# Kernel tuning notes

Measured on AMD Instinct MI355X. Metric: run time of the kernel, lower is better.

## Reference

```python
import jax, jax.numpy as jnp
import numpy as np

S = 3        # message passing steps
L = 128      # latent size
N = 10000    # nodes
E = 160000   # edges
DN, DE, DG = 64, 16, 8
OUT = 8
EPS = 1e-5


def _ln(x, scale, offset):
    m = jnp.mean(x, axis=-1, keepdims=True)
    v = jnp.var(x, axis=-1, keepdims=True)
    return (x - m) * jax.lax.rsqrt(v + EPS) * scale + offset


def _mlp(x, W0, b0, W1, b1):
    h = jax.nn.relu(x @ W0 + b0)
    return jax.nn.relu(h @ W1 + b1)


def setup_inputs() -> dict:
    key = jax.random.key(0)
    ks = iter(jax.random.split(key, 64))

    def w(shape, fan_in):
        return jax.random.normal(next(ks), shape, jnp.float32) / np.sqrt(fan_in).astype(np.float32)

    inp = {
        "nodes": jax.random.normal(next(ks), (N, DN), jnp.float32),
        "edges": jax.random.normal(next(ks), (E, DE), jnp.float32),
        "globals_": jax.random.normal(next(ks), (1, DG), jnp.float32),
        "senders": jax.random.randint(next(ks), (E,), 0, N),
        "receivers": jax.random.randint(next(ks), (E,), 0, N),
        # embedder
        "emb_node_W": w((DN, L), DN), "emb_node_b": jnp.zeros((L,), jnp.float32),
        "emb_edge_W": w((DE, L), DE), "emb_edge_b": jnp.zeros((L,), jnp.float32),
        "emb_glob_W": w((DG, L), DG), "emb_glob_b": jnp.zeros((L,), jnp.float32),
        # per-step MLPs (2 layers each)
        "edge_W0": w((S, 4 * L, L), 4 * L), "edge_b0": jnp.zeros((S, L), jnp.float32),
        "edge_W1": w((S, L, L), L),         "edge_b1": jnp.zeros((S, L), jnp.float32),
        "node_W0": w((S, 4 * L, L), 4 * L), "node_b0": jnp.zeros((S, L), jnp.float32),
        "node_W1": w((S, L, L), L),         "node_b1": jnp.zeros((S, L), jnp.float32),
        "glob_W0": w((S, 3 * L, L), 3 * L), "glob_b0": jnp.zeros((S, L), jnp.float32),
        "glob_W1": w((S, L, L), L),         "glob_b1": jnp.zeros((S, L), jnp.float32),
        # per-step layernorm (0: nodes, 1: edges, 2: globals)
        "ln_scale": jnp.ones((S, 3, L), jnp.float32),
        "ln_offset": jnp.zeros((S, 3, L), jnp.float32),
        # decoder (globals only)
        "dec_W": w((L, OUT), L), "dec_b": jnp.zeros((OUT,), jnp.float32),
    }
    return inp


def reference(nodes, edges, globals_, senders, receivers,
              emb_node_W, emb_node_b, emb_edge_W, emb_edge_b, emb_glob_W, emb_glob_b,
              edge_W0, edge_b0, edge_W1, edge_b1,
              node_W0, node_b0, node_W1, node_b1,
              glob_W0, glob_b0, glob_W1, glob_b1,
              ln_scale, ln_offset, dec_W, dec_b):
    # embed to latent
    n = nodes @ emb_node_W + emb_node_b      # [N, L]
    e = edges @ emb_edge_W + emb_edge_b      # [E, L]
    g = globals_ @ emb_glob_W + emb_glob_b   # [1, L]

    for s in range(S):
        # edge update: concat(edges, nodes[senders], nodes[receivers], globals)
        g_e = jnp.broadcast_to(g, (e.shape[0], L))
        e_in = jnp.concatenate([e, n[senders], n[receivers], g_e], axis=-1)  # [E, 4L]
        e_new = _mlp(e_in, edge_W0[s], edge_b0[s], edge_W1[s], edge_b1[s])
        # node update: concat(nodes, segsum(e,senders), segsum(e,receivers), globals)
        sent_agg = jax.ops.segment_sum(e_new, senders, num_segments=N)
        recv_agg = jax.ops.segment_sum(e_new, receivers, num_segments=N)
        g_n = jnp.broadcast_to(g, (N, L))
        n_in = jnp.concatenate([n, sent_agg, recv_agg, g_n], axis=-1)  # [N, 4L]
        n_new = _mlp(n_in, node_W0[s], node_b0[s], node_W1[s], node_b1[s])
        # global update: concat(node_agg, edge_agg, globals) (single graph)
        node_agg = jnp.sum(n_new, axis=0, keepdims=True)
        edge_agg = jnp.sum(e_new, axis=0, keepdims=True)
        g_in = jnp.concatenate([node_agg, edge_agg, g], axis=-1)  # [1, 3L]
        g_new = _mlp(g_in, glob_W0[s], glob_b0[s], glob_W1[s], glob_b1[s])
        # residual + layernorm
        n = _ln(n_new + n, ln_scale[s, 0], ln_offset[s, 0])
        e = _ln(e_new + e, ln_scale[s, 1], ln_offset[s, 1])
        g = _ln(g_new + g, ln_scale[s, 2], ln_offset[s, 2])

    # decoder maps globals only
    return g @ dec_W + dec_b  # [1, OUT]
```

## Files before the change

### kernel.cpp

```cpp
#include <hip/hip_runtime.h>
#include <hip/hip_bf16.h>

typedef __bf16 bf16;
typedef __bf16 bf16x8 __attribute__((ext_vector_type(8)));
typedef __bf16 bf16x4 __attribute__((ext_vector_type(4)));
typedef float  f32x4  __attribute__((ext_vector_type(4)));

#define NL 128
#define NN 10000
#define NE 160000
#define LN_EPS 1e-5f

__device__ __forceinline__ f32x4 f4zero() {
    f32x4 v; v[0] = 0.f; v[1] = 0.f; v[2] = 0.f; v[3] = 0.f; return v;
}

__device__ __forceinline__ int swz_off(int row, int b) {
    return row * 256 + (b ^ ((row & 7) << 4));
}

__device__ __forceinline__ bf16x8 frag_ld(const bf16* base, int row, int kbyte) {
    return *reinterpret_cast<const bf16x8*>(
        reinterpret_cast<const char*>(base) + swz_off(row, kbyte));
}

template <int NT>
__device__ __forceinline__ void stage_img(const bf16* __restrict__ img, bf16* dst, int tid) {
    #pragma unroll
    for (int i = 0; i < 2048 / NT; ++i) {
        int byte = (i * NT + tid) * 16;
        *reinterpret_cast<bf16x8*>(reinterpret_cast<char*>(dst) + byte) =
            *reinterpret_cast<const bf16x8*>(reinterpret_cast<const char*>(img) + byte);
    }
}

template <int NT>
__device__ __forceinline__ void stage_img_ld(const bf16* __restrict__ img, bf16x8* r, int tid) {
    #pragma unroll
    for (int i = 0; i < 2048 / NT; ++i)
        r[i] = *reinterpret_cast<const bf16x8*>(reinterpret_cast<const char*>(img) +
                                                (i * NT + tid) * 16);
}
template <int NT>
__device__ __forceinline__ void stage_img_st(bf16* dst, const bf16x8* r, int tid) {
    #pragma unroll
    for (int i = 0; i < 2048 / NT; ++i)
        *reinterpret_cast<bf16x8*>(reinterpret_cast<char*>(dst) + (i * NT + tid) * 16) = r[i];
}

__device__ __forceinline__ void stage_rows16(const float* __restrict__ src0, bf16* sX,
                                             int wrow0, int lane) {
    int c8 = (lane & 15) * 8;
    #pragma unroll
    for (int i = 0; i < 4; ++i) {
        int sub = i * 4 + (lane >> 4);
        const float* src = src0 + (size_t)sub * 128 + c8;
        f32x4 a = *reinterpret_cast<const f32x4*>(src);
        f32x4 b = *reinterpret_cast<const f32x4*>(src + 4);
        bf16x8 v;
        v[0] = (bf16)a[0]; v[1] = (bf16)a[1]; v[2] = (bf16)a[2]; v[3] = (bf16)a[3];
        v[4] = (bf16)b[0]; v[5] = (bf16)b[1]; v[6] = (bf16)b[2]; v[7] = (bf16)b[3];
        *reinterpret_cast<bf16x8*>(reinterpret_cast<char*>(sX) + swz_off(wrow0 + sub, c8 * 2)) = v;
    }
}

__device__ __forceinline__ void mfma_16x128(const bf16* sA, const bf16* sB, int arow, int kq,
                                            f32x4 acc[8]) {
    #pragma unroll
    for (int kk = 0; kk < 4; ++kk) {
        bf16x8 af = frag_ld(sA, arow, kk * 64 + kq);
        #pragma unroll
        for (int t = 0; t < 8; ++t) {
            bf16x8 bfr = frag_ld(sB, t * 16 + (arow & 15), kk * 64 + kq);
            acc[t] = __builtin_amdgcn_mfma_f32_16x16x32_bf16(af, bfr, acc[t], 0, 0, 0);
        }
    }
}

__device__ __forceinline__ void acc_to_lds_bf16(bf16* sX, const f32x4 acc[8], int w, int lane) {
    int c0 = lane & 15;
    #pragma unroll
    for (int r = 0; r < 4; ++r) {
        int rl = w * 16 + (lane >> 4) * 4 + r;
        #pragma unroll
        for (int t = 0; t < 8; ++t) {
            int col = t * 16 + c0;
            *reinterpret_cast<bf16*>(reinterpret_cast<char*>(sX) + swz_off(rl, col * 2)) =
                (bf16)acc[t][r];
        }
    }
}

__device__ __forceinline__ void lds_rows_to_global_bf16(const bf16* sX, bf16* __restrict__ dst0,
                                                        int w, int lane) {
    int c8 = (lane & 15) * 8;
    #pragma unroll
    for (int i = 0; i < 4; ++i) {
        int sub = i * 4 + (lane >> 4);
        bf16x8 v = *reinterpret_cast<const bf16x8*>(
            reinterpret_cast<const char*>(sX) + swz_off(w * 16 + sub, c8 * 2));
        *reinterpret_cast<bf16x8*>(dst0 + (size_t)sub * 128 + c8) = v;
    }
}

__global__ void k_prep(const float* __restrict__ eW0, const float* __restrict__ eW1,
                       const float* __restrict__ nW0, const float* __restrict__ nW1,
                       bf16* __restrict__ imgs, const float* __restrict__ globals_,
                       const float* __restrict__ embW, const float* __restrict__ embB,
                       float* __restrict__ g, const float* __restrict__ eb0,
                       const float* __restrict__ nb0, float* __restrict__ gve,
                       float* __restrict__ gvn, int* __restrict__ deg,
                       float* __restrict__ eagg, float* __restrict__ nagg,
                       int* __restrict__ done) {
    const int b = blockIdx.x;
    const int tid = threadIdx.x;
    if (b < 24) {
        const int s = b >> 3, kind = b & 7;
        const float* src;
        if (kind < 3)       src = eW0 + (size_t)s * 512 * 128 + (size_t)kind * 128 * 128;
        else if (kind == 3) src = eW1 + (size_t)s * 128 * 128;
        else if (kind < 7)  src = nW0 + (size_t)s * 512 * 128 + (size_t)(kind - 4) * 128 * 128;
        else                src = nW1 + (size_t)s * 128 * 128;
        bf16* img = imgs + (size_t)b * 16384;
        for (int i = 0; i < 16; ++i) {
            int q = tid + i * 256;
            int col = q & 127;
            int k0 = (q >> 7) << 2;
            bf16x4 v;
            v[0] = (bf16)src[(k0 + 0) * 128 + col];
            v[1] = (bf16)src[(k0 + 1) * 128 + col];
            v[2] = (bf16)src[(k0 + 2) * 128 + col];
            v[3] = (bf16)src[(k0 + 3) * 128 + col];
            *reinterpret_cast<bf16x4*>(reinterpret_cast<char*>(img) + swz_off(col, k0 * 2)) = v;
        }
    } else if (b == 24) {
        __shared__ float sG[128];
        if (tid < 3) done[tid] = 0;
        if (tid < 128) {
            float a = embB[tid];
            #pragma unroll
            for (int k = 0; k < 8; ++k) a += globals_[k] * embW[k * 128 + tid];
            g[tid] = a;
            sG[tid] = a;
        }
        __syncthreads();
        if (tid < 128) {
            const float* eW0g = eW0 + 384 * 128;
            const float* nW0g = nW0 + 384 * 128;
            float ae = eb0[tid], an = nb0[tid];
            for (int k = 0; k < 128; ++k) {
                float gv = sG[k];
                ae += gv * eW0g[k * 128 + tid];
                an += gv * nW0g[k * 128 + tid];
            }
            gve[tid] = ae;
            gvn[tid] = an;
        }
    } else {
        for (int i = tid; i < 2 * NN; i += 256) deg[i] = 0;
        for (int i = tid; i < 8 * 128; i += 256) eagg[i] = 0.f;
        for (int i = tid; i < 4 * 128; i += 256) nagg[i] = 0.f;
    }
}


__global__ void k_hist(const int* __restrict__ senders, const int* __restrict__ receivers,
                       int* __restrict__ deg_s, int* __restrict__ deg_r) {
    int i = blockIdx.x * 256 + threadIdx.x;
    if (i < NE) {
        atomicAdd(&deg_s[senders[i]], 1);
        atomicAdd(&deg_r[receivers[i]], 1);
    }
}

__device__ void scan_arr(const int* __restrict__ deg, int* __restrict__ rs, int* __restrict__ cur,
                         int* sW, int* sRun) {
    const int tid = threadIdx.x, lane = tid & 63, wid = tid >> 6;
    if (tid == 0) *sRun = 0;
    __syncthreads();
    for (int base = 0; base < NN; base += 1024) {
        int i = base + tid;
        int orig = (i < NN) ? deg[i] : 0;
        int v = orig;
        #pragma unroll
        for (int off = 1; off < 64; off <<= 1) {
            int u = __shfl_up(v, off, 64);
            if (lane >= off) v += u;
        }
        if (lane == 63) sW[wid] = v;
        __syncthreads();
        if (wid == 0 && lane < 16) {
            int u = sW[lane];
            #pragma unroll
            for (int off = 1; off < 16; off <<= 1) {
                int t = __shfl_up(u, off, 16);
                if (lane >= off) u += t;
            }
            sW[lane] = u;
        }
        __syncthreads();
        int waveoff = (wid == 0) ? 0 : sW[wid - 1];
        int incl = v + waveoff + *sRun;
        if (i < NN) {
            rs[i + 1] = incl;
            cur[i] = incl - orig;
        }
        __syncthreads();
        if (tid == 1023) *sRun = incl;
        __syncthreads();
    }
    if (tid == 0) rs[0] = 0;
}

__global__ void k_scan(const int* __restrict__ deg_s, int* __restrict__ rs_s,
                       int* __restrict__ cur_s, const int* __restrict__ deg_r,
                       int* __restrict__ rs_r, int* __restrict__ cur_r) {
    __shared__ int sW[16];
    __shared__ int sRun;
    scan_arr(deg_s, rs_s, cur_s, sW, &sRun);
    __syncthreads();
    scan_arr(deg_r, rs_r, cur_r, sW, &sRun);
}

__global__ void k_scatter_s(const int* __restrict__ senders, const int* __restrict__ receivers,
                            int* __restrict__ cur_s, int* __restrict__ perm,
                            int* __restrict__ snd_s, int* __restrict__ rcv_s) {
    int i = blockIdx.x * 256 + threadIdx.x;
    if (i < NE) {
        int s = senders[i];
        int p = atomicAdd(&cur_s[s], 1);
        perm[p] = i;
        snd_s[p] = s;
        rcv_s[p] = receivers[i];
    }
}

__global__ void k_scatter_r(const int* __restrict__ rcv_s, int* __restrict__ cur_r,
                            int* __restrict__ csr_r) {
    int j = blockIdx.x * 256 + threadIdx.x;
    if (j < NE) {
        int r = rcv_s[j];
        int p = atomicAdd(&cur_r[r], 1);
        csr_r[p] = j;
    }
}


__global__ __launch_bounds__(256, 2) void k_embed_nodes(
    const float* __restrict__ nodes, const float* __restrict__ W, const float* __restrict__ b,
    float* __restrict__ n_out, const bf16* __restrict__ imgPs, const bf16* __restrict__ imgPr,
    bf16* __restrict__ nsW, bf16* __restrict__ nrW) {
    __shared__ __align__(16) char smem[81920];
    float* sWemb = (float*)smem;
    float* sB = (float*)(smem + 32768);
    bf16* sWa = (bf16*)smem;
    bf16* sWb = (bf16*)(smem + 32768);
    bf16* sX = (bf16*)(smem + 65536);
    const int tid = threadIdx.x;
    const int lane = tid & 63;
    const int w = tid >> 6;
    const int rowbase = blockIdx.x * 64;
    const bool wvalid = (rowbase + w * 16) < NN;

    for (int i = tid; i < 64 * 128; i += 256) sWemb[i] = W[i];
    if (tid < 128) sB[tid] = b[tid];
    __syncthreads();

    const int rg = tid >> 4;
    const int c8 = (tid & 15) * 8;
    #pragma unroll
    for (int p = 0; p < 4; ++p) {
        int row = rowbase + p * 16 + rg;
        if (row < NN) {
            const f32x4* x4 = reinterpret_cast<const f32x4*>(nodes + (size_t)row * 64);
            float o[8];
            #pragma unroll
            for (int j = 0; j < 8; ++j) o[j] = sB[c8 + j];
            #pragma unroll
            for (int k4 = 0; k4 < 16; ++k4) {
                f32x4 xv = x4[k4];
                #pragma unroll
                for (int kk = 0; kk < 4; ++kk) {
                    float x = xv[kk];
                    const float* wrow = sWemb + (k4 * 4 + kk) * 128 + c8;
                    f32x4 wA = *reinterpret_cast<const f32x4*>(wrow);
                    f32x4 wB = *reinterpret_cast<const f32x4*>(wrow + 4);
                    o[0] += x * wA[0]; o[1] += x * wA[1]; o[2] += x * wA[2]; o[3] += x * wA[3];
                    o[4] += x * wB[0]; o[5] += x * wB[1]; o[6] += x * wB[2]; o[7] += x * wB[3];
                }
            }
            f32x4 oA, oB;
            bf16x8 v;
            #pragma unroll
            for (int j = 0; j < 8; ++j) {
                if (j < 4) oA[j] = o[j]; else oB[j - 4] = o[j];
                v[j] = (bf16)o[j];
            }
            float* orow = n_out + (size_t)row * 128 + c8;
            *reinterpret_cast<f32x4*>(orow) = oA;
            *reinterpret_cast<f32x4*>(orow + 4) = oB;
            *reinterpret_cast<bf16x8*>(reinterpret_cast<char*>(sX) +
                                       swz_off(p * 16 + rg, c8 * 2)) = v;
        }
    }
    __syncthreads();
    stage_img<256>(imgPs, sWa, tid);
    stage_img<256>(imgPr, sWb, tid);
    __syncthreads();
    if (!wvalid) return;

    const int arow = w * 16 + (lane & 15);
    const int kq = (lane >> 4) * 16;
    f32x4 acc[8], acc2[8];
    #pragma unroll
    for (int t = 0; t < 8; ++t) { acc[t] = f4zero(); acc2[t] = f4zero(); }
    mfma_16x128(sX, sWa, arow, kq, acc);
    mfma_16x128(sX, sWb, arow, kq, acc2);

    acc_to_lds_bf16(sX, acc, w, lane);
    lds_rows_to_global_bf16(sX, nsW + (size_t)(rowbase + w * 16) * 128, w, lane);
    acc_to_lds_bf16(sX, acc2, w, lane);
    lds_rows_to_global_bf16(sX, nrW + (size_t)(rowbase + w * 16) * 128, w, lane);
}

__global__ __launch_bounds__(256) void k_embed_edges(const float* __restrict__ edges,
                                                     const int* __restrict__ perm,
                                                     const float* __restrict__ W,
                                                     const float* __restrict__ b,
                                                     bf16* __restrict__ e_out) {
    __shared__ float sW[16 * 128];
    __shared__ float sB[128];
    const int tid = threadIdx.x;
    for (int i = tid; i < 16 * 128; i += 256) sW[i] = W[i];
    if (tid < 128) sB[tid] = b[tid];
    __syncthreads();
    const int rg = tid >> 4;
    const int c8 = (tid & 15) * 8;
    const int rowbase = blockIdx.x * 128;
    #pragma unroll 2
    for (int p = 0; p < 8; ++p) {
        int row = rowbase + p * 16 + rg;
        int src = perm[row];
        const f32x4* x4 = reinterpret_cast<const f32x4*>(edges + (size_t)src * 16);
        f32x4 xr[4] = {x4[0], x4[1], x4[2], x4[3]};
        float o[8];
        #pragma unroll
        for (int j = 0; j < 8; ++j) o[j] = sB[c8 + j];
        #pragma unroll
        for (int q = 0; q < 4; ++q) {
            #pragma unroll
            for (int kk = 0; kk < 4; ++kk) {
                float x = xr[q][kk];
                const float* wrow = sW + (q * 4 + kk) * 128 + c8;
                f32x4 wA = *reinterpret_cast<const f32x4*>(wrow);
                f32x4 wB = *reinterpret_cast<const f32x4*>(wrow + 4);
                o[0] += x * wA[0]; o[1] += x * wA[1]; o[2] += x * wA[2]; o[3] += x * wA[3];
                o[4] += x * wB[0]; o[5] += x * wB[1]; o[6] += x * wB[2]; o[7] += x * wB[3];
            }
        }
        bf16x8 v;
        #pragma unroll
        for (int j = 0; j < 8; ++j) v[j] = (bf16)o[j];
        *reinterpret_cast<bf16x8*>(e_out + (size_t)row * 128 + c8) = v;
    }
}


__global__ __launch_bounds__(512, 2) void k_edge(
    bf16* e_rw, bf16* __restrict__ e_new_out, const bf16* __restrict__ nsW,
    const bf16* __restrict__ nrW, float* __restrict__ edge_agg,
    const int* __restrict__ snd_s, const int* __restrict__ rcv_s,
    const bf16* __restrict__ imgW0, const bf16* __restrict__ imgW1,
    const float* __restrict__ gvec, const float* __restrict__ b1,
    const float* __restrict__ lnS, const float* __restrict__ lnO) {
    __shared__ __align__(16) char smem[65536];
    bf16* sW = (bf16*)smem;
    bf16* sX = (bf16*)(smem + 32768);
    float* sEagg = (float*)smem;

    const int tid = threadIdx.x;
    const int lane = tid & 63;
    const int w = tid >> 6;
    const int rowbase = blockIdx.x * 128;
    const int arow = w * 16 + (lane & 15);
    const int kq = (lane >> 4) * 16;
    const int c0 = lane & 15;
    const int qrt = lane >> 4;
    const int c8 = c0 * 8;

    stage_img<512>(imgW0, sW, tid);

    int snd_i[4], rcv_i[4];
    bf16x8 eold8[4];
    #pragma unroll
    for (int i = 0; i < 4; ++i) {
        int gr = rowbase + w * 16 + i * 4 + qrt;
        snd_i[i] = snd_s[gr];
        rcv_i[i] = rcv_s[gr];
        eold8[i] = *reinterpret_cast<const bf16x8*>(e_rw + (size_t)gr * 128 + c8);
    }

    f32x4 gvA = *reinterpret_cast<const f32x4*>(gvec + c8);
    f32x4 gvB = *reinterpret_cast<const f32x4*>(gvec + c8 + 4);
    f32x4 lsA = *reinterpret_cast<const f32x4*>(lnS + c8);
    f32x4 lsB = *reinterpret_cast<const f32x4*>(lnS + c8 + 4);
    f32x4 loA = *reinterpret_cast<const f32x4*>(lnO + c8);
    f32x4 loB = *reinterpret_cast<const f32x4*>(lnO + c8 + 4);
    float bb[8];
    #pragma unroll
    for (int t = 0; t < 8; ++t) bb[t] = b1[t * 16 + c0];

    bf16x8 ns8[4], nr8[4];
    #pragma unroll
    for (int i = 0; i < 4; ++i) {
        ns8[i] = *reinterpret_cast<const bf16x8*>(nsW + (size_t)snd_i[i] * 128 + c8);
        nr8[i] = *reinterpret_cast<const bf16x8*>(nrW + (size_t)rcv_i[i] * 128 + c8);
    }

    #pragma unroll
    for (int i = 0; i < 4; ++i)
        *reinterpret_cast<bf16x8*>(reinterpret_cast<char*>(sX) +
                                   swz_off(w * 16 + i * 4 + qrt, c8 * 2)) = eold8[i];

    __syncthreads();

    f32x4 acc[8];
    #pragma unroll
    for (int t = 0; t < 8; ++t) acc[t] = f4zero();
    __builtin_amdgcn_s_setprio(1);
    mfma_16x128(sX, sW, arow, kq, acc);
    __builtin_amdgcn_s_setprio(0);

    __syncthreads();

    bf16x8 w1r[4];
    stage_img_ld<512>(imgW1, w1r, tid);

    #pragma unroll
    for (int r = 0; r < 4; ++r) {
        int rl = w * 16 + (lane >> 4) * 4 + r;
        #pragma unroll
        for (int t = 0; t < 8; ++t)
            *reinterpret_cast<bf16*>(reinterpret_cast<char*>(sX) +
                                     swz_off(rl, (t * 16 + c0) * 2)) = (bf16)acc[t][r];
    }
    #pragma unroll
    for (int i = 0; i < 4; ++i) {
        int rl = w * 16 + i * 4 + qrt;
        bf16x8 a8 = *reinterpret_cast<const bf16x8*>(
            reinterpret_cast<const char*>(sX) + swz_off(rl, c8 * 2));
        bf16x8 h8;
        #pragma unroll
        for (int j = 0; j < 8; ++j) {
            float gvj = (j < 4) ? gvA[j] : gvB[j - 4];
            float v = (float)a8[j] + (float)ns8[i][j] + (float)nr8[i][j] + gvj;
            h8[j] = (bf16)fmaxf(v, 0.f);
        }
        *reinterpret_cast<bf16x8*>(reinterpret_cast<char*>(sX) + swz_off(rl, c8 * 2)) = h8;
    }

    stage_img_st<512>(sW, w1r, tid);
    __syncthreads();

    f32x4 acc2[8];
    #pragma unroll
    for (int t = 0; t < 8; ++t) acc2[t] = f4zero();
    __builtin_amdgcn_s_setprio(1);
    mfma_16x128(sX, sW, arow, kq, acc2);
    __builtin_amdgcn_s_setprio(0);

    #pragma unroll
    for (int r = 0; r < 4; ++r) {
        int rl = w * 16 + (lane >> 4) * 4 + r;
        #pragma unroll
        for (int t = 0; t < 8; ++t)
            *reinterpret_cast<bf16*>(reinterpret_cast<char*>(sX) +
                                     swz_off(rl, (t * 16 + c0) * 2)) =
                (bf16)fmaxf(acc2[t][r] + bb[t], 0.f);
    }

    float cs[8];
    #pragma unroll
    for (int j = 0; j < 8; ++j) cs[j] = 0.f;
    bf16* enew0 = e_new_out + (size_t)rowbase * 128;
    bf16* e0 = e_rw + (size_t)rowbase * 128;
    #pragma unroll
    for (int i = 0; i < 4; ++i) {
        int sub = w * 16 + i * 4 + qrt;
        bf16x8 en8 = *reinterpret_cast<const bf16x8*>(
            reinterpret_cast<const char*>(sX) + swz_off(sub, c8 * 2));
        *reinterpret_cast<bf16x8*>(enew0 + (size_t)sub * 128 + c8) = en8;
        float rv[8], s1 = 0.f, s2 = 0.f;
        #pragma unroll
        for (int j = 0; j < 8; ++j) {
            float en = (float)en8[j];
            cs[j] += en;
            float v = en + (float)eold8[i][j];
            rv[j] = v;
            s1 += v;
            s2 += v * v;
        }
        #pragma unroll
        for (int off = 1; off < 16; off <<= 1) {
            s1 += __shfl_xor(s1, off, 16);
            s2 += __shfl_xor(s2, off, 16);
        }
        float mean = s1 * (1.f / 128.f);
        float rstd = rsqrtf(s2 * (1.f / 128.f) - mean * mean + LN_EPS);
        bf16x8 o8;
        #pragma unroll
        for (int j = 0; j < 8; ++j) {
            float ls = (j < 4) ? lsA[j] : lsB[j - 4];
            float lo = (j < 4) ? loA[j] : loB[j - 4];
            o8[j] = (bf16)((rv[j] - mean) * rstd * ls + lo);
        }
        *reinterpret_cast<bf16x8*>(e0 + (size_t)sub * 128 + c8) = o8;
    }

    #pragma unroll
    for (int j = 0; j < 8; ++j) {
        cs[j] += __shfl_xor(cs[j], 16, 64);
        cs[j] += __shfl_xor(cs[j], 32, 64);
    }
    __syncthreads();
    if (qrt == 0) {
        float* dst = sEagg + w * 128 + c8;
        #pragma unroll
        for (int j = 0; j < 8; ++j) dst[j] = cs[j];
    }
    __syncthreads();
    if (tid < 128) {
        float v = 0.f;
        #pragma unroll
        for (int ww = 0; ww < 8; ++ww) v += sEagg[ww * 128 + tid];
        atomicAdd(&edge_agg[(blockIdx.x & 7) * 128 + tid], v);
    }
}

__global__ __launch_bounds__(256) void k_agg(const bf16* __restrict__ e_new,
                                             const int* __restrict__ rs_s,
                                             const int* __restrict__ rs_r,
                                             const int* __restrict__ csr_r,
                                             bf16* __restrict__ sent, bf16* __restrict__ recv) {
    const int lane = threadIdx.x & 63;
    const int w = threadIdx.x >> 6;
    const int node = blockIdx.x * 4 + w;
    if (node >= NN) return;
    const int qrt = lane >> 4;
    const int c8 = (lane & 15) * 8;
    float a[8];
    #pragma unroll
    for (int j = 0; j < 8; ++j) a[j] = 0.f;
    const int b0 = rs_s[node], b1 = rs_s[node + 1];
    for (int jj = b0 + qrt; jj < b1; jj += 4) {
        bf16x8 v = *reinterpret_cast<const bf16x8*>(e_new + (size_t)jj * 128 + c8);
        #pragma unroll
        for (int j = 0; j < 8; ++j) a[j] += (float)v[j];
    }
    #pragma unroll
    for (int j = 0; j < 8; ++j) {
        a[j] += __shfl_xor(a[j], 16, 64);
        a[j] += __shfl_xor(a[j], 32, 64);
    }
    if (qrt == 0) {
        bf16x8 o;
        #pragma unroll
        for (int j = 0; j < 8; ++j) o[j] = (bf16)a[j];
        *reinterpret_cast<bf16x8*>(sent + (size_t)node * 128 + c8) = o;
    }
    #pragma unroll
    for (int j = 0; j < 8; ++j) a[j] = 0.f;
    const int c1 = rs_r[node], c2 = rs_r[node + 1];
    for (int pp = c1 + qrt; pp < c2; pp += 4) {
        int jj = csr_r[pp];
        bf16x8 v = *reinterpret_cast<const bf16x8*>(e_new + (size_t)jj * 128 + c8);
        #pragma unroll
        for (int j = 0; j < 8; ++j) a[j] += (float)v[j];
    }
    #pragma unroll
    for (int j = 0; j < 8; ++j) {
        a[j] += __shfl_xor(a[j], 16, 64);
        a[j] += __shfl_xor(a[j], 32, 64);
    }
    if (qrt == 0) {
        bf16x8 o;
        #pragma unroll
        for (int j = 0; j < 8; ++j) o[j] = (bf16)a[j];
        *reinterpret_cast<bf16x8*>(recv + (size_t)node * 128 + c8) = o;
    }
}

__global__ __launch_bounds__(256, 2) void k_node(
    float* n_rw, const bf16* __restrict__ sent, const bf16* __restrict__ recv,
    float* __restrict__ node_agg , const bf16* __restrict__ imgW0,
    const bf16* __restrict__ imgW1, const float* __restrict__ gvec,
    const float* __restrict__ b1, const float* __restrict__ lnS,
    const float* __restrict__ lnO, const bf16* __restrict__ imgPs,
    const bf16* __restrict__ imgPr, bf16* __restrict__ nsW, bf16* __restrict__ nrW,
    int do_proj,
    int* __restrict__ done_ctr, float* __restrict__ edge_agg , float* __restrict__ g,
    const float* __restrict__ gW0, const float* __restrict__ gb0,
    const float* __restrict__ gW1, const float* __restrict__ gb1,
    const float* __restrict__ glnS, const float* __restrict__ glnO,
    const float* __restrict__ eW0g, const float* __restrict__ eb0n,
    const float* __restrict__ nW0g, const float* __restrict__ nb0n,
    float* __restrict__ gve, float* __restrict__ gvn, const float* __restrict__ decW,
    const float* __restrict__ decb, float* __restrict__ out, int do_next, int do_dec) {
    __shared__ __align__(16) char smem[81920];
    __shared__ int sLast;
    bf16* sA = (bf16*)smem;
    bf16* sB = (bf16*)(smem + 32768);
    bf16* sX = (bf16*)(smem + 65536);
    float* sNagg = (float*)smem;

    const int tid = threadIdx.x;
    const int lane = tid & 63;
    const int w = tid >> 6;
    const int rowbase = blockIdx.x * 64;
    const bool wvalid = (rowbase + w * 16) < NN;
    const int arow = w * 16 + (lane & 15);
    const int kq = (lane >> 4) * 16;
    const int c0 = lane & 15;
    const int qrt = lane >> 4;
    const int c8 = c0 * 8;

    stage_img<256>(imgW0, sA, tid);
    stage_img<256>(imgW0 + 16384, sB, tid);
    bf16x8 sent8[4], recv8[4];
    if (wvalid) {
        stage_rows16(n_rw + (size_t)(rowbase + w * 16) * 128, sX, w * 16, lane);
        #pragma unroll
        for (int i = 0; i < 4; ++i) {
            int gr = rowbase + w * 16 + i * 4 + qrt;
            sent8[i] = *reinterpret_cast<const bf16x8*>(sent + (size_t)gr * 128 + c8);
            recv8[i] = *reinterpret_cast<const bf16x8*>(recv + (size_t)gr * 128 + c8);
        }
    }
    __syncthreads();

    float gvf[8], bbf[8];
    #pragma unroll
    for (int t = 0; t < 8; ++t) {
        gvf[t] = gvec[t * 16 + c0];
        bbf[t] = b1[t * 16 + c0];
    }
    f32x4 lsA4 = *reinterpret_cast<const f32x4*>(lnS + c8);
    f32x4 lsB4 = *reinterpret_cast<const f32x4*>(lnS + c8 + 4);
    f32x4 loA4 = *reinterpret_cast<const f32x4*>(lnO + c8);
    f32x4 loB4 = *reinterpret_cast<const f32x4*>(lnO + c8 + 4);

    f32x4 acc[8];
    #pragma unroll
    for (int t = 0; t < 8; ++t) acc[t] = f4zero();
    float cs[8];
    #pragma unroll
    for (int j = 0; j < 8; ++j) cs[j] = 0.f;

    if (wvalid) mfma_16x128(sX, sA, arow, kq, acc);
    __syncthreads();

    stage_img<256>(imgW0 + 32768, sA, tid);
    if (wvalid) {
        #pragma unroll
        for (int i = 0; i < 4; ++i)
            *reinterpret_cast<bf16x8*>(reinterpret_cast<char*>(sX) +
                                       swz_off(w * 16 + i * 4 + qrt, c8 * 2)) = sent8[i];
        mfma_16x128(sX, sB, arow, kq, acc);
    }
    __syncthreads();

    stage_img<256>(imgW1, sB, tid);
    if (wvalid) {
        #pragma unroll
        for (int i = 0; i < 4; ++i)
            *reinterpret_cast<bf16x8*>(reinterpret_cast<char*>(sX) +
                                       swz_off(w * 16 + i * 4 + qrt, c8 * 2)) = recv8[i];
        mfma_16x128(sX, sA, arow, kq, acc);

        #pragma unroll
        for (int r = 0; r < 4; ++r) {
            int rl = w * 16 + (lane >> 4) * 4 + r;
            #pragma unroll
            for (int t = 0; t < 8; ++t)
                *reinterpret_cast<bf16*>(reinterpret_cast<char*>(sX) +
                                         swz_off(rl, (t * 16 + c0) * 2)) =
                    (bf16)fmaxf(acc[t][r] + gvf[t], 0.f);
        }
    }
    __syncthreads();

    if (wvalid) {
        #pragma unroll
        for (int t = 0; t < 8; ++t) acc[t] = f4zero();
        mfma_16x128(sX, sB, arow, kq, acc);
        #pragma unroll
        for (int r = 0; r < 4; ++r) {
            int rl = w * 16 + (lane >> 4) * 4 + r;
            #pragma unroll
            for (int t = 0; t < 8; ++t)
                *reinterpret_cast<bf16*>(reinterpret_cast<char*>(sX) +
                                         swz_off(rl, (t * 16 + c0) * 2)) =
                    (bf16)fmaxf(acc[t][r] + bbf[t], 0.f);
        }

        const float* nbase = n_rw + (size_t)(rowbase + w * 16) * 128;
        #pragma unroll
        for (int i = 0; i < 4; ++i) {
            int sub = i * 4 + qrt;
            bf16x8 en8 = *reinterpret_cast<const bf16x8*>(
                reinterpret_cast<const char*>(sX) + swz_off(w * 16 + sub, c8 * 2));
            f32x4 noA = *reinterpret_cast<const f32x4*>(nbase + (size_t)sub * 128 + c8);
            f32x4 noB = *reinterpret_cast<const f32x4*>(nbase + (size_t)sub * 128 + c8 + 4);
            float rv[8], s1 = 0.f, s2 = 0.f;
            #pragma unroll
            for (int j = 0; j < 8; ++j) {
                float en = (float)en8[j];
                cs[j] += en;
                float v = en + ((j < 4) ? noA[j] : noB[j - 4]);
                rv[j] = v;
                s1 += v;
                s2 += v * v;
            }
            #pragma unroll
            for (int off = 1; off < 16; off <<= 1) {
                s1 += __shfl_xor(s1, off, 16);
                s2 += __shfl_xor(s2, off, 16);
            }
            float mean = s1 * (1.f / 128.f);
            float rstd = rsqrtf(s2 * (1.f / 128.f) - mean * mean + LN_EPS);
            f32x4 oA, oB;
            bf16x8 l8;
            #pragma unroll
            for (int j = 0; j < 8; ++j) {
                float ls = (j < 4) ? lsA4[j] : lsB4[j - 4];
                float lo = (j < 4) ? loA4[j] : loB4[j - 4];
                float o = (rv[j] - mean) * rstd * ls + lo;
                if (j < 4) oA[j] = o; else oB[j - 4] = o;
                l8[j] = (bf16)o;
            }
            float* orow = n_rw + (size_t)(rowbase + w * 16 + sub) * 128 + c8;
            *reinterpret_cast<f32x4*>(orow) = oA;
            *reinterpret_cast<f32x4*>(orow + 4) = oB;
            *reinterpret_cast<bf16x8*>(reinterpret_cast<char*>(sX) +
                                       swz_off(w * 16 + sub, c8 * 2)) = l8;
        }
    }

    if (do_proj) {
        __syncthreads();
        stage_img<256>(imgPs, sA, tid);
        stage_img<256>(imgPr, sB, tid);
        __syncthreads();
        if (wvalid) {
            f32x4 pa[8], pb[8];
            #pragma unroll
            for (int t = 0; t < 8; ++t) { pa[t] = f4zero(); pb[t] = f4zero(); }
            mfma_16x128(sX, sA, arow, kq, pa);
            mfma_16x128(sX, sB, arow, kq, pb);
            acc_to_lds_bf16(sX, pa, w, lane);
            lds_rows_to_global_bf16(sX, nsW + (size_t)(rowbase + w * 16) * 128, w, lane);
            acc_to_lds_bf16(sX, pb, w, lane);
            lds_rows_to_global_bf16(sX, nrW + (size_t)(rowbase + w * 16) * 128, w, lane);
        }
    }

    #pragma unroll
    for (int j = 0; j < 8; ++j) {
        cs[j] += __shfl_xor(cs[j], 16, 64);
        cs[j] += __shfl_xor(cs[j], 32, 64);
    }
    __syncthreads();
    if (qrt == 0) {
        float* dst = sNagg + w * 128 + c8;
        #pragma unroll
        for (int j = 0; j < 8; ++j) dst[j] = wvalid ? cs[j] : 0.f;
    }
    __syncthreads();
    if (tid < 128) {
        float v = sNagg[tid] + sNagg[128 + tid] + sNagg[256 + tid] + sNagg[384 + tid];
        atomicAdd(&node_agg[(blockIdx.x & 3) * 128 + tid], v);
    }

    __syncthreads();
    if (tid == 0) {
        __threadfence();
        int old = atomicAdd(done_ctr, 1);
        sLast = (old == (int)gridDim.x - 1);
    }
    __syncthreads();
    if (!sLast) return;

    float* sIn = (float*)smem;
    float* sP0 = sIn + 384;
    float* sP1 = sP0 + 128;
    float* sH = sP1 + 128;
    float* sG = sH + 128;
    float* sMR = sG + 128;
    const int j = tid & 127;
    const int part = tid >> 7;

    if (tid < 128) {
        float v = 0.f;
        #pragma unroll
        for (int c = 0; c < 4; ++c) v += atomicAdd(&node_agg[c * 128 + tid], 0.f);
        #pragma unroll
        for (int c = 0; c < 4; ++c) atomicExch(&node_agg[c * 128 + tid], 0.f);
        sIn[tid] = v;
        sIn[256 + tid] = g[tid];
    } else {
        float v = 0.f;
        #pragma unroll
        for (int c = 0; c < 8; ++c) v += edge_agg[c * 128 + j];
        #pragma unroll
        for (int c = 0; c < 8; ++c) edge_agg[c * 128 + j] = 0.f;
        sIn[128 + j] = v;
    }
    __syncthreads();
    {
        float p = 0.f;
        for (int k = 0; k < 192; ++k) {
            int kk = part * 192 + k;
            p += sIn[kk] * gW0[(size_t)kk * 128 + j];
        }
        (part ? sP1 : sP0)[j] = p;
    }
    __syncthreads();
    if (tid < 128) sH[tid] = fmaxf(gb0[tid] + sP0[tid] + sP1[tid], 0.f);
    __syncthreads();
    {
        float p = 0.f;
        for (int k = 0; k < 64; ++k) {
            int kk = part * 64 + k;
            p += sH[kk] * gW1[(size_t)kk * 128 + j];
        }
        (part ? sP1 : sP0)[j] = p;
    }
    __syncthreads();
    float res = 0.f;
    if (tid < 128) {
        res = fmaxf(gb1[tid] + sP0[tid] + sP1[tid], 0.f) + sIn[256 + tid];
        sP0[tid] = res;
        sP1[tid] = res * res;
    }
    __syncthreads();
    if (tid < 64) {
        float a = sP0[tid] + sP0[tid + 64];
        float q = sP1[tid] + sP1[tid + 64];
        #pragma unroll
        for (int off = 1; off < 64; off <<= 1) {
            a += __shfl_xor(a, off, 64);
            q += __shfl_xor(q, off, 64);
        }
        if (tid == 0) {
            float m = a * (1.f / 128.f);
            float v = q * (1.f / 128.f) - m * m;
            sMR[0] = m;
            sMR[1] = rsqrtf(v + LN_EPS);
        }
    }
    __syncthreads();
    if (tid < 128) {
        float go = (res - sMR[0]) * sMR[1] * glnS[tid] + glnO[tid];
        g[tid] = go;
        sG[tid] = go;
    }
    __syncthreads();
    if (do_next) {
        float pe = 0.f, pn = 0.f;
        for (int k = 0; k < 64; ++k) {
            int kk = part * 64 + k;
            float gv = sG[kk];
            pe += gv * eW0g[(size_t)kk * 128 + j];
            pn += gv * nW0g[(size_t)kk * 128 + j];
        }
        (part ? sP1 : sP0)[j] = pe;
        sIn[part * 128 + j] = pn;
        __syncthreads();
        if (tid < 128) {
            gve[tid] = eb0n[tid] + sP0[tid] + sP1[tid];
            gvn[tid] = nb0n[tid] + sIn[tid] + sIn[128 + tid];
        }
    }
    if (do_dec && tid < 8) {
        float a = decb[tid];
        for (int k = 0; k < 128; ++k) a += sG[k] * decW[k * 8 + tid];
        out[tid] = a;
    }
}

extern "C" void kernel_launch(void* const* d_in, const int* in_sizes, int n_in, void* d_out,
                              int out_size, void* d_ws, size_t ws_size, hipStream_t stream) {
    (void)in_sizes; (void)n_in; (void)out_size; (void)ws_size;
    const float* nodes = (const float*)d_in[0];
    const float* edges = (const float*)d_in[1];
    const float* globals_ = (const float*)d_in[2];
    const int* senders = (const int*)d_in[3];
    const int* receivers = (const int*)d_in[4];
    const float* emb_node_W = (const float*)d_in[5];
    const float* emb_node_b = (const float*)d_in[6];
    const float* emb_edge_W = (const float*)d_in[7];
    const float* emb_edge_b = (const float*)d_in[8];
    const float* emb_glob_W = (const float*)d_in[9];
    const float* emb_glob_b = (const float*)d_in[10];
    const float* edge_W0 = (const float*)d_in[11];
    const float* edge_b0 = (const float*)d_in[12];
    const float* edge_W1 = (const float*)d_in[13];
    const float* edge_b1 = (const float*)d_in[14];
    const float* node_W0 = (const float*)d_in[15];
    const float* node_b0 = (const float*)d_in[16];
    const float* node_W1 = (const float*)d_in[17];
    const float* node_b1 = (const float*)d_in[18];
    const float* glob_W0 = (const float*)d_in[19];
    const float* glob_b0 = (const float*)d_in[20];
    const float* glob_W1 = (const float*)d_in[21];
    const float* glob_b1 = (const float*)d_in[22];
    const float* ln_scale = (const float*)d_in[23];
    const float* ln_offset = (const float*)d_in[24];
    const float* dec_W = (const float*)d_in[25];
    const float* dec_b = (const float*)d_in[26];

    char* ws = (char*)d_ws;
    size_t off = 0;
    auto alloc = [&](size_t bytes) -> char* {
        char* p = ws + off;
        off += (bytes + 255) & ~(size_t)255;
        return p;
    };
    bf16* e = (bf16*)alloc((size_t)NE * NL * 2);
    bf16* e_new = (bf16*)alloc((size_t)NE * NL * 2);
    float* n = (float*)alloc((size_t)NN * NL * 4);
    bf16* nsW = (bf16*)alloc((size_t)NN * NL * 2);
    bf16* nrW = (bf16*)alloc((size_t)NN * NL * 2);
    bf16* sent = (bf16*)alloc((size_t)NN * NL * 2);
    bf16* recv = (bf16*)alloc((size_t)NN * NL * 2);
    bf16* imgs = (bf16*)alloc((size_t)24 * 16384 * 2);
    float* eagg = (float*)alloc(8 * 128 * 4);
    float* nagg = (float*)alloc(4 * 128 * 4);
    float* g = (float*)alloc(128 * 4);
    float* gve = (float*)alloc(128 * 4);
    float* gvn = (float*)alloc(128 * 4);
    int* done = (int*)alloc(16 * 4);
    int* deg = (int*)alloc((size_t)2 * NN * 4);
    int* deg_s = deg;
    int* deg_r = deg + NN;
    int* rs_s = (int*)alloc((size_t)(NN + 1) * 4);
    int* rs_r = (int*)alloc((size_t)(NN + 1) * 4);
    int* cur_s = (int*)alloc((size_t)NN * 4);
    int* cur_r = (int*)alloc((size_t)NN * 4);
    int* perm = (int*)alloc((size_t)NE * 4);
    int* snd_s = (int*)alloc((size_t)NE * 4);
    int* rcv_s = (int*)alloc((size_t)NE * 4);
    int* csr_r = (int*)alloc((size_t)NE * 4);

    const int NB_N = (NN + 63) / 64;
    const int NB_E = NE / 128;
    const int NB_EMB = NE / 128;
    const int NB_SC = (NE + 255) / 256;
    const int NB_AGG = NN / 4;

    auto img = [&](int s, int kind) -> const bf16* {
        return imgs + ((size_t)s * 8 + kind) * 16384;
    };

    k_prep<<<26, 256, 0, stream>>>(edge_W0, edge_W1, node_W0, node_W1, imgs, globals_,
                                   emb_glob_W, emb_glob_b, g, edge_b0, node_b0, gve, gvn,
                                   deg, eagg, nagg, done);

    k_hist<<<NB_SC, 256, 0, stream>>>(senders, receivers, deg_s, deg_r);
    k_scan<<<1, 1024, 0, stream>>>(deg_s, rs_s, cur_s, deg_r, rs_r, cur_r);
    k_scatter_s<<<NB_SC, 256, 0, stream>>>(senders, receivers, cur_s, perm, snd_s, rcv_s);
    k_scatter_r<<<NB_SC, 256, 0, stream>>>(rcv_s, cur_r, csr_r);

    k_embed_nodes<<<NB_N, 256, 0, stream>>>(nodes, emb_node_W, emb_node_b, n, img(0, 1),
                                            img(0, 2), nsW, nrW);
    k_embed_edges<<<NB_EMB, 256, 0, stream>>>(edges, perm, emb_edge_W, emb_edge_b, e);

    for (int s = 0; s < 3; ++s) {
        const int last = (s == 2);
        k_edge<<<NB_E, 512, 0, stream>>>(e, e_new, nsW, nrW, eagg, snd_s, rcv_s, img(s, 0),
                                         img(s, 3), gve, edge_b1 + s * 128,
                                         ln_scale + (s * 3 + 1) * 128,
                                         ln_offset + (s * 3 + 1) * 128);
        k_agg<<<NB_AGG, 256, 0, stream>>>(e_new, rs_s, rs_r, csr_r, sent, recv);
        const float* eW0g = last ? edge_W0 : edge_W0 + (size_t)(s + 1) * 512 * 128 + 384 * 128;
        const float* eb0n = last ? edge_b0 : edge_b0 + (s + 1) * 128;
        const float* nW0g = last ? node_W0 : node_W0 + (size_t)(s + 1) * 512 * 128 + 384 * 128;
        const float* nb0n = last ? node_b0 : node_b0 + (s + 1) * 128;
        k_node<<<NB_N, 256, 0, stream>>>(
            n, sent, recv, nagg, img(s, 4), img(s, 7), gvn, node_b1 + s * 128,
            ln_scale + (s * 3 + 0) * 128, ln_offset + (s * 3 + 0) * 128,
            img(last ? 0 : s + 1, 1), img(last ? 0 : s + 1, 2), nsW, nrW, !last,
            done + s, eagg, g, glob_W0 + (size_t)s * 384 * 128, glob_b0 + s * 128,
            glob_W1 + (size_t)s * 128 * 128, glob_b1 + s * 128, ln_scale + (s * 3 + 2) * 128,
            ln_offset + (s * 3 + 2) * 128, eW0g, eb0n, nW0g, nb0n, gve, gvn, dec_W, dec_b,
            (float*)d_out, !last, last);
    }
}
```

Before: 400.4 us.

## Read edge MLP weights as MFMA fragments from global instead of staging in LDS

Adds a prep step that stores the edge MLP weights pre-arranged in MFMA B-fragment order, so each lane reads its fragment straight from global memory (through L2 and cache) rather than staging a 32KB weight tile in LDS. The edge kernel shrinks to 256 threads handling 64 rows per block, with far less LDS and fewer block-wide barriers, which should allow more resident blocks and better latency hiding. The cost is that every wave now fetches the full weight matrices from global or cache, so performance depends on cache hit rates.

```diff
diff --git a/kernel.cpp b/kernel.cpp
--- a/kernel.cpp
+++ b/kernel.cpp
@@ -32,20 +32,6 @@
         *reinterpret_cast<bf16x8*>(reinterpret_cast<char*>(dst) + byte) =
             *reinterpret_cast<const bf16x8*>(reinterpret_cast<const char*>(img) + byte);
     }
-}
-
-template <int NT>
-__device__ __forceinline__ void stage_img_ld(const bf16* __restrict__ img, bf16x8* r, int tid) {
-    #pragma unroll
-    for (int i = 0; i < 2048 / NT; ++i)
-        r[i] = *reinterpret_cast<const bf16x8*>(reinterpret_cast<const char*>(img) +
-                                                (i * NT + tid) * 16);
-}
-template <int NT>
-__device__ __forceinline__ void stage_img_st(bf16* dst, const bf16x8* r, int tid) {
-    #pragma unroll
-    for (int i = 0; i < 2048 / NT; ++i)
-        *reinterpret_cast<bf16x8*>(reinterpret_cast<char*>(dst) + (i * NT + tid) * 16) = r[i];
 }
 
 __device__ __forceinline__ void stage_rows16(const float* __restrict__ src0, bf16* sX,
@@ -77,6 +63,20 @@
     }
 }
 
+__device__ __forceinline__ void mfma_16x128g(const bf16* sA, const bf16* __restrict__ imgB,
+                                             int arow, int kq, int lane, f32x4 acc[8]) {
+    #pragma unroll
+    for (int kk = 0; kk < 4; ++kk) {
+        bf16x8 af = frag_ld(sA, arow, kk * 64 + kq);
+        #pragma unroll
+        for (int t = 0; t < 8; ++t) {
+            bf16x8 bfr = *reinterpret_cast<const bf16x8*>(
+                imgB + (size_t)(((kk * 8 + t) * 64 + lane)) * 8);
+            acc[t] = __builtin_amdgcn_mfma_f32_16x16x32_bf16(af, bfr, acc[t], 0, 0, 0);
+        }
+    }
+}
+
 __device__ __forceinline__ void acc_to_lds_bf16(bf16* sX, const f32x4 acc[8], int w, int lane) {
     int c0 = lane & 15;
     #pragma unroll
@@ -105,7 +105,8 @@
 
 __global__ void k_prep(const float* __restrict__ eW0, const float* __restrict__ eW1,
                        const float* __restrict__ nW0, const float* __restrict__ nW1,
-                       bf16* __restrict__ imgs, const float* __restrict__ globals_,
+                       bf16* __restrict__ imgs, bf16* __restrict__ fimgs,
+                       const float* __restrict__ globals_,
                        const float* __restrict__ embW, const float* __restrict__ embB,
                        float* __restrict__ g, const float* __restrict__ eb0,
                        const float* __restrict__ nb0, float* __restrict__ gve,
@@ -133,7 +134,25 @@
             v[3] = (bf16)src[(k0 + 3) * 128 + col];
             *reinterpret_cast<bf16x4*>(reinterpret_cast<char*>(img) + swz_off(col, k0 * 2)) = v;
         }
-    } else if (b == 24) {
+    } else if (b < 30) {
+        const int f = b - 24, s = f >> 1, which = f & 1;
+        const float* src = which ? (eW1 + (size_t)s * 128 * 128)
+                                 : (eW0 + (size_t)s * 512 * 128);
+        bf16* img = fimgs + (size_t)f * 16384;
+        #pragma unroll
+        for (int i = 0; i < 8; ++i) {
+            int q = tid + i * 256;
+            int l = q & 63;
+            int ft = q >> 6;
+            int kk = ft >> 3, t = ft & 7;
+            int col = t * 16 + (l & 15);
+            int k0 = kk * 32 + (l >> 4) * 8;
+            bf16x8 v;
+            #pragma unroll
+            for (int j = 0; j < 8; ++j) v[j] = (bf16)src[(size_t)(k0 + j) * 128 + col];
+            *reinterpret_cast<bf16x8*>(img + (size_t)q * 8) = v;
+        }
+    } else if (b == 30) {
         __shared__ float sG[128];
         if (tid < 3) done[tid] = 0;
         if (tid < 128) {
@@ -366,30 +385,27 @@
 }
 
 
-__global__ __launch_bounds__(512, 2) void k_edge(
+__global__ __launch_bounds__(256) void k_edge(
     bf16* e_rw, bf16* __restrict__ e_new_out, const bf16* __restrict__ nsW,
     const bf16* __restrict__ nrW, float* __restrict__ edge_agg,
     const int* __restrict__ snd_s, const int* __restrict__ rcv_s,
-    const bf16* __restrict__ imgW0, const bf16* __restrict__ imgW1,
+    const bf16* __restrict__ fimgW0, const bf16* __restrict__ fimgW1,
     const float* __restrict__ gvec, const float* __restrict__ b1,
     const float* __restrict__ lnS, const float* __restrict__ lnO) {
-    __shared__ __align__(16) char smem[65536];
-    bf16* sW = (bf16*)smem;
-    bf16* sX = (bf16*)(smem + 32768);
-    float* sEagg = (float*)smem;
+    __shared__ __align__(16) char smem[18432];
+    bf16* sX = (bf16*)smem;
+    float* sEagg = (float*)(smem + 16384);
 
     const int tid = threadIdx.x;
     const int lane = tid & 63;
     const int w = tid >> 6;
-    const int rowbase = blockIdx.x * 128;
+    const int rowbase = blockIdx.x * 64;
     const int arow = w * 16 + (lane & 15);
     const int kq = (lane >> 4) * 16;
     const int c0 = lane & 15;
     const int qrt = lane >> 4;
     const int c8 = c0 * 8;
 
-    stage_img<512>(imgW0, sW, tid);
-
     int snd_i[4], rcv_i[4];
     bf16x8 eold8[4];
     #pragma unroll
@@ -399,46 +415,30 @@
         rcv_i[i] = rcv_s[gr];
         eold8[i] = *reinterpret_cast<const bf16x8*>(e_rw + (size_t)gr * 128 + c8);
     }
-
-    f32x4 gvA = *reinterpret_cast<const f32x4*>(gvec + c8);
-    f32x4 gvB = *reinterpret_cast<const f32x4*>(gvec + c8 + 4);
-    f32x4 lsA = *reinterpret_cast<const f32x4*>(lnS + c8);
-    f32x4 lsB = *reinterpret_cast<const f32x4*>(lnS + c8 + 4);
-    f32x4 loA = *reinterpret_cast<const f32x4*>(lnO + c8);
-    f32x4 loB = *reinterpret_cast<const f32x4*>(lnO + c8 + 4);
-    float bb[8];
-    #pragma unroll
-    for (int t = 0; t < 8; ++t) bb[t] = b1[t * 16 + c0];
-
     bf16x8 ns8[4], nr8[4];
     #pragma unroll
     for (int i = 0; i < 4; ++i) {
         ns8[i] = *reinterpret_cast<const bf16x8*>(nsW + (size_t)snd_i[i] * 128 + c8);
         nr8[i] = *reinterpret_cast<const bf16x8*>(nrW + (size_t)rcv_i[i] * 128 + c8);
     }
+    f32x4 gvA = *reinterpret_cast<const f32x4*>(gvec + c8);
+    f32x4 gvB = *reinterpret_cast<const f32x4*>(gvec + c8 + 4);
 
     #pragma unroll
     for (int i = 0; i < 4; ++i)
         *reinterpret_cast<bf16x8*>(reinterpret_cast<char*>(sX) +
                                    swz_off(w * 16 + i * 4 + qrt, c8 * 2)) = eold8[i];
 
-    __syncthreads();
-
     f32x4 acc[8];
     #pragma unroll
     for (int t = 0; t < 8; ++t) acc[t] = f4zero();
     __builtin_amdgcn_s_setprio(1);
-    mfma_16x128(sX, sW, arow, kq, acc);
+    mfma_16x128g(sX, fimgW0, arow, kq, lane, acc);
     __builtin_amdgcn_s_setprio(0);
 
-    __syncthreads();
-
-    bf16x8 w1r[4];
-    stage_img_ld<512>(imgW1, w1r, tid);
-
     #pragma unroll
     for (int r = 0; r < 4; ++r) {
-        int rl = w * 16 + (lane >> 4) * 4 + r;
+        int rl = w * 16 + qrt * 4 + r;
         #pragma unroll
         for (int t = 0; t < 8; ++t)
             *reinterpret_cast<bf16*>(reinterpret_cast<char*>(sX) +
@@ -459,19 +459,24 @@
         *reinterpret_cast<bf16x8*>(reinterpret_cast<char*>(sX) + swz_off(rl, c8 * 2)) = h8;
     }
 
-    stage_img_st<512>(sW, w1r, tid);
-    __syncthreads();
-
     f32x4 acc2[8];
     #pragma unroll
     for (int t = 0; t < 8; ++t) acc2[t] = f4zero();
     __builtin_amdgcn_s_setprio(1);
-    mfma_16x128(sX, sW, arow, kq, acc2);
+    mfma_16x128g(sX, fimgW1, arow, kq, lane, acc2);
     __builtin_amdgcn_s_setprio(0);
 
+    float bb[8];
+    #pragma unroll
+    for (int t = 0; t < 8; ++t) bb[t] = b1[t * 16 + c0];
+    f32x4 lsA = *reinterpret_cast<const f32x4*>(lnS + c8);
+    f32x4 lsB = *reinterpret_cast<const f32x4*>(lnS + c8 + 4);
+    f32x4 loA = *reinterpret_cast<const f32x4*>(lnO + c8);
+    f32x4 loB = *reinterpret_cast<const f32x4*>(lnO + c8 + 4);
+
     #pragma unroll
     for (int r = 0; r < 4; ++r) {
-        int rl = w * 16 + (lane >> 4) * 4 + r;
+        int rl = w * 16 + qrt * 4 + r;
         #pragma unroll
         for (int t = 0; t < 8; ++t)
             *reinterpret_cast<bf16*>(reinterpret_cast<char*>(sX) +
@@ -530,9 +535,7 @@
     }
     __syncthreads();
     if (tid < 128) {
-        float v = 0.f;
-        #pragma unroll
-        for (int ww = 0; ww < 8; ++ww) v += sEagg[ww * 128 + tid];
+        float v = sEagg[tid] + sEagg[128 + tid] + sEagg[256 + tid] + sEagg[384 + tid];
         atomicAdd(&edge_agg[(blockIdx.x & 7) * 128 + tid], v);
     }
 }
@@ -934,6 +937,7 @@
     bf16* sent = (bf16*)alloc((size_t)NN * NL * 2);
     bf16* recv = (bf16*)alloc((size_t)NN * NL * 2);
     bf16* imgs = (bf16*)alloc((size_t)24 * 16384 * 2);
+    bf16* fimgs = (bf16*)alloc((size_t)6 * 16384 * 2);
     float* eagg = (float*)alloc(8 * 128 * 4);
     float* nagg = (float*)alloc(4 * 128 * 4);
     float* g = (float*)alloc(128 * 4);
@@ -953,7 +957,7 @@
     int* csr_r = (int*)alloc((size_t)NE * 4);
 
     const int NB_N = (NN + 63) / 64;
-    const int NB_E = NE / 128;
+    const int NB_E = NE / 64;
     const int NB_EMB = NE / 128;
     const int NB_SC = (NE + 255) / 256;
     const int NB_AGG = NN / 4;
@@ -961,8 +965,11 @@
     auto img = [&](int s, int kind) -> const bf16* {
         return imgs + ((size_t)s * 8 + kind) * 16384;
     };
-
-    k_prep<<<26, 256, 0, stream>>>(edge_W0, edge_W1, node_W0, node_W1, imgs, globals_,
+    auto fimg = [&](int s, int which) -> const bf16* {
+        return fimgs + ((size_t)s * 2 + which) * 16384;
+    };
+
+    k_prep<<<32, 256, 0, stream>>>(edge_W0, edge_W1, node_W0, node_W1, imgs, fimgs, globals_,
                                    emb_glob_W, emb_glob_b, g, edge_b0, node_b0, gve, gvn,
                                    deg, eagg, nagg, done);
 
@@ -977,8 +984,8 @@
 
     for (int s = 0; s < 3; ++s) {
         const int last = (s == 2);
-        k_edge<<<NB_E, 512, 0, stream>>>(e, e_new, nsW, nrW, eagg, snd_s, rcv_s, img(s, 0),
-                                         img(s, 3), gve, edge_b1 + s * 128,
+        k_edge<<<NB_E, 256, 0, stream>>>(e, e_new, nsW, nrW, eagg, snd_s, rcv_s, fimg(s, 0),
+                                         fimg(s, 1), gve, edge_b1 + s * 128,
                                          ln_scale + (s * 3 + 1) * 128,
                                          ln_offset + (s * 3 + 1) * 128);
         k_agg<<<NB_AGG, 256, 0, stream>>>(e_new, rs_s, rs_r, csr_r, sent, recv);
```

New measurement: 461.5 us. +15.3%, slower.
